# Kernel tuning notes

Hardware: AMD Instinct MI355X
Metric: run time of the kernel (lower is better)

Reference implementation:

```python
import jax, jax.numpy as jnp
import numpy as np

N = 100000
E = 800000
IN_DIM = 256
H = 4
C = 32          # per-head hidden dim
SLOPE = 0.2


def gat_conv(x, W, att_src, att_dst, bias, src, dst):
    """PyG GATConv (single input tensor => lin_src applied to both src and dst),
    concat=True, add_self_loops=False, eval mode (no attn dropout).
    x: [N, F_in], W: [H*C, F_in], att_src/att_dst: [H, C], bias: [H*C].
    Returns [N, H*C]."""
    n = x.shape[0]
    xp = (x @ W.T).reshape(n, H, C)                    # [N,H,C]
    a_src = jnp.einsum('nhc,hc->nh', xp, att_src)      # [N,H]
    a_dst = jnp.einsum('nhc,hc->nh', xp, att_dst)      # [N,H]
    e = a_src[src] + a_dst[dst]                        # [E,H]
    e = jax.nn.leaky_relu(e, SLOPE)
    # segment softmax over incoming edges of each dst node
    m = jax.ops.segment_max(e, dst, num_segments=n)    # [N,H]
    ex = jnp.exp(e - m[dst])                           # [E,H]
    s = jax.ops.segment_sum(ex, dst, num_segments=n)   # [N,H]
    alpha = ex / (s[dst] + 1e-16)                      # [E,H]
    msg = xp[src] * alpha[:, :, None]                  # [E,H,C]
    out = jax.ops.segment_sum(msg, dst, num_segments=n)  # [N,H,C]
    return out.reshape(n, H * C) + bias


def setup_inputs() -> dict:
    key = jax.random.key(0)
    ks = jax.random.split(key, 12)
    x = jax.random.normal(ks[0], (N, IN_DIM), dtype=jnp.float32)
    edge_index = jax.random.randint(ks[1], (2, E), 0, N, dtype=jnp.int64)
    g = 1.414

    def xavier(k, shape):
        fan_in, fan_out = shape[-1], int(np.prod(shape[:-1]))
        std = g * np.sqrt(2.0 / (fan_in + fan_out))
        return jax.random.normal(k, shape, dtype=jnp.float32) * std

    W0 = xavier(ks[2], (H * C, IN_DIM))
    att_src0 = xavier(ks[3], (H, C))
    att_dst0 = xavier(ks[4], (H, C))
    b0 = jnp.zeros((H * C,), dtype=jnp.float32)
    W1 = xavier(ks[5], (H * C, H * C))
    att_src1 = xavier(ks[6], (H, C))
    att_dst1 = xavier(ks[7], (H, C))
    b1 = jnp.zeros((H * C,), dtype=jnp.float32)
    return {"x": x, "edge_index": edge_index,
            "W0": W0, "att_src0": att_src0, "att_dst0": att_dst0, "b0": b0,
            "W1": W1, "att_src1": att_src1, "att_dst1": att_dst1, "b1": b1}


def reference(x, edge_index, W0, att_src0, att_dst0, b0, W1, att_src1, att_dst1, b1):
    src, dst = edge_index[0], edge_index[1]
    h = gat_conv(x, W0, att_src0, att_dst0, b0, src, dst)
    h = jax.nn.relu(h)                 # activation on all but last layer
    h = gat_conv(h, W1, att_src1, att_dst1, b1, src, dst)
    # encoding=False => no last activation; head is Identity
    return h
```

## Files before the change

### kernel.cpp

```cpp
#include <hip/hip_runtime.h>
#include <hip/hip_bf16.h>
#include <cstdint>
#include <cstddef>
#include <type_traits>

#define SLOPE 0.2f

typedef __attribute__((ext_vector_type(8))) short short8v;
typedef __attribute__((ext_vector_type(4))) float float4v;

__device__ inline ushort f2bf(float f) {
  uint u = __float_as_uint(f);
  uint r = (u + 0x7FFFu + ((u >> 16) & 1u)) >> 16;
  return (ushort)r;
}
__device__ inline float bf2f(ushort u) {
  return __uint_as_float(((uint)u) << 16);
}
__device__ inline float bflo(uint u) { return __uint_as_float(u << 16); }
__device__ inline float bfhi(uint u) { return __uint_as_float(u & 0xffff0000u); }

__device__ inline short8v pack8(float4 a, float4 b) {
  uint4 r;
  r.x = (uint)f2bf(a.x) | ((uint)f2bf(a.y) << 16);
  r.y = (uint)f2bf(a.z) | ((uint)f2bf(a.w) << 16);
  r.z = (uint)f2bf(b.x) | ((uint)f2bf(b.y) << 16);
  r.w = (uint)f2bf(b.z) | ((uint)f2bf(b.w) << 16);
  return __builtin_bit_cast(short8v, r);
}


__global__ void k_wconv(const float* __restrict__ W0, const float* __restrict__ W1,
                        ushort* __restrict__ Wb0, ushort* __restrict__ Wb1) {
  int i = blockIdx.x * 256 + threadIdx.x;
  if (i < 128 * 256) Wb0[i] = f2bf(W0[i]);
  if (i < 128 * 128) Wb1[i] = f2bf(W1[i]);
}


__global__ void k_count(const int* __restrict__ dst, int* __restrict__ counts, int E) {
  int e = blockIdx.x * 256 + threadIdx.x;
  if (e < E) atomicAdd(&counts[dst[e]], 1);
}

__global__ void k_scan1(const int* __restrict__ counts, int* __restrict__ excl,
                        int* __restrict__ bsums, int N) {
  __shared__ int lds[256];
  int tid = threadIdx.x;
  int base = blockIdx.x * 2048 + tid * 8;
  int v[8];
  int ts = 0;
#pragma unroll
  for (int i = 0; i < 8; i++) {
    int idx = base + i;
    int t = (idx < N) ? counts[idx] : 0;
    v[i] = ts;
    ts += t;
  }
  lds[tid] = ts;
  __syncthreads();
  for (int off = 1; off < 256; off <<= 1) {
    int t = (tid >= off) ? lds[tid - off] : 0;
    __syncthreads();
    lds[tid] += t;
    __syncthreads();
  }
  int texcl = (tid > 0) ? lds[tid - 1] : 0;
#pragma unroll
  for (int i = 0; i < 8; i++) {
    int idx = base + i;
    if (idx < N) excl[idx] = texcl + v[i];
  }
  if (tid == 255) bsums[blockIdx.x] = lds[255];
}

__global__ void k_scan2(int* bsums, int nb) {
  __shared__ int lds[256];
  int tid = threadIdx.x;
  int v = (tid < nb) ? bsums[tid] : 0;
  lds[tid] = v;
  __syncthreads();
  for (int off = 1; off < 256; off <<= 1) {
    int t = (tid >= off) ? lds[tid - off] : 0;
    __syncthreads();
    lds[tid] += t;
    __syncthreads();
  }
  if (tid < nb) bsums[tid] = (tid > 0) ? lds[tid - 1] : 0;
}

__global__ void k_scan3(int* __restrict__ excl, int* __restrict__ cursor,
                        const int* __restrict__ bsums, int N) {
  int tid = threadIdx.x;
  int off = bsums[blockIdx.x];
  int base = blockIdx.x * 2048 + tid * 8;
#pragma unroll
  for (int i = 0; i < 8; i++) {
    int idx = base + i;
    if (idx < N) {
      int val = excl[idx] + off;
      excl[idx] = val;
      cursor[idx] = val;
    }
  }
}

__global__ void k_fill(const int* __restrict__ src, const int* __restrict__ dst,
                       int* __restrict__ cursor,
                       int* __restrict__ src_sorted, int* __restrict__ dst_sorted,
                       int E) {
  int e = blockIdx.x * 256 + threadIdx.x;
  if (e < E) {
    int d = dst[e];
    int pos = atomicAdd(&cursor[d], 1);
    src_sorted[pos] = src[e];
    dst_sorted[pos] = d;
  }
}


template <typename AT, int K>
__global__ __launch_bounds__(256, 2) void k_gemm_lds(
    const AT* __restrict__ A, const ushort* __restrict__ Wb,
    const float* __restrict__ att_src, const float* __restrict__ att_dst,
    ushort* __restrict__ C, float* __restrict__ a_src, float* __restrict__ a_dst,
    int M) {
  constexpr int LDW = K + 8;
  __shared__ ushort Ws[128 * LDW];
  const int tid = threadIdx.x;
  const int wave = tid >> 6, lane = tid & 63;
  const int fr = lane & 15, fq = lane >> 4;
  const int bm = blockIdx.x * 128;
  const int r0 = bm + wave * 32 + fr;
  const int r1 = r0 + 16;
  const int rc0 = min(r0, M - 1), rc1 = min(r1, M - 1);

  {
    int r = tid >> 1, cb = (tid & 1) * (K / 2);
    const ushort* wp = Wb + (size_t)r * K + cb;
    ushort* dp = &Ws[r * LDW + cb];
#pragma unroll
    for (int i = 0; i < K / 16; i++)
      *(uint4*)(dp + i * 8) = *(const uint4*)(wp + i * 8);
  }
  __syncthreads();

  float4v acc[2][8] = {};
#pragma unroll
  for (int k0 = 0; k0 < K; k0 += 32) {
    short8v af0, af1;
    if constexpr (std::is_same<AT, float>::value) {
      const float* p0 = A + (size_t)rc0 * K + k0 + fq * 8;
      const float* p1 = A + (size_t)rc1 * K + k0 + fq * 8;
      af0 = pack8(*(const float4*)p0, *(const float4*)(p0 + 4));
      af1 = pack8(*(const float4*)p1, *(const float4*)(p1 + 4));
    } else {
      af0 = *(const short8v*)(A + (size_t)rc0 * K + k0 + fq * 8);
      af1 = *(const short8v*)(A + (size_t)rc1 * K + k0 + fq * 8);
    }
    short8v bfr[8];
#pragma unroll
    for (int t = 0; t < 8; t++)
      bfr[t] = *(const short8v*)&Ws[(t * 16 + fr) * LDW + k0 + fq * 8];
#pragma unroll
    for (int t = 0; t < 8; t++)
      acc[0][t] = __builtin_amdgcn_mfma_f32_16x16x32_bf16(af0, bfr[t], acc[0][t], 0, 0, 0);
#pragma unroll
    for (int t = 0; t < 8; t++)
      acc[1][t] = __builtin_amdgcn_mfma_f32_16x16x32_bf16(af1, bfr[t], acc[1][t], 0, 0, 0);
  }

  float asc[8], adc[8];
#pragma unroll
  for (int t = 0; t < 8; t++) {
    asc[t] = att_src[t * 16 + fr];
    adc[t] = att_dst[t * 16 + fr];
  }

#pragma unroll
  for (int s = 0; s < 2; s++) {
#pragma unroll
    for (int j = 0; j < 4; j++) {
      int row = bm + wave * 32 + s * 16 + fq * 4 + j;
      bool ok = row < M;
      if (ok) {
#pragma unroll
        for (int t = 0; t < 8; t++)
          C[(size_t)row * 128 + t * 16 + fr] = f2bf(acc[s][t][j]);
      }
      float ps[4], pd[4];
#pragma unroll
      for (int h = 0; h < 4; h++) {
        ps[h] = acc[s][2 * h][j] * asc[2 * h] + acc[s][2 * h + 1][j] * asc[2 * h + 1];
        pd[h] = acc[s][2 * h][j] * adc[2 * h] + acc[s][2 * h + 1][j] * adc[2 * h + 1];
      }
#pragma unroll
      for (int off = 1; off < 16; off <<= 1) {
#pragma unroll
        for (int h = 0; h < 4; h++) {
          ps[h] += __shfl_xor(ps[h], off);
          pd[h] += __shfl_xor(pd[h], off);
        }
      }
      if (ok && fr == 0) {
        *(float4*)&a_src[(size_t)row * 4] = make_float4(ps[0], ps[1], ps[2], ps[3]);
        *(float4*)&a_dst[(size_t)row * 4] = make_float4(pd[0], pd[1], pd[2], pd[3]);
      }
    }
  }
}


__global__ void k_edge(const int* __restrict__ ss, const int* __restrict__ ds,
                       const float* __restrict__ a_src, const float* __restrict__ a_dst,
                       float* __restrict__ e_sorted, int E) {
  int p = blockIdx.x * 256 + threadIdx.x;
  if (p >= E) return;
  int s = ss[p], d = ds[p];
  float4 as4 = *(const float4*)&a_src[s * 4];
  float4 ad4 = *(const float4*)&a_dst[d * 4];
  float4 ev;
  ev.x = as4.x + ad4.x; ev.x = (ev.x > 0.f) ? ev.x : SLOPE * ev.x;
  ev.y = as4.y + ad4.y; ev.y = (ev.y > 0.f) ? ev.y : SLOPE * ev.y;
  ev.z = as4.z + ad4.z; ev.z = (ev.z > 0.f) ? ev.z : SLOPE * ev.z;
  ev.w = as4.w + ad4.w; ev.w = (ev.w > 0.f) ? ev.w : SLOPE * ev.w;
  *(float4*)&e_sorted[p * 4] = ev;
}


__global__ __launch_bounds__(256) void k_msum(const float* __restrict__ e_sorted,
                                              const int* __restrict__ indptr,
                                              const int* __restrict__ counts,
                                              float* __restrict__ m_buf,
                                              float* __restrict__ inv_buf, int N) {
  int t = blockIdx.x * 256 + threadIdx.x;
  int n = t >> 2, h = t & 3;
  if (n >= N) return;
  int deg = counts[n], start = indptr[n];
  const float* eb = e_sorted + (size_t)start * 4 + h;
  float m0 = -INFINITY, m1 = -INFINITY, m2 = -INFINITY, m3 = -INFINITY;
  int i = 0;
  for (; i + 4 <= deg; i += 4) {
    float a = eb[(i + 0) * 4], b = eb[(i + 1) * 4];
    float c = eb[(i + 2) * 4], d = eb[(i + 3) * 4];
    m0 = fmaxf(m0, a); m1 = fmaxf(m1, b); m2 = fmaxf(m2, c); m3 = fmaxf(m3, d);
  }
  for (; i < deg; i++) m0 = fmaxf(m0, eb[i * 4]);
  float m = fmaxf(fmaxf(m0, m1), fmaxf(m2, m3));
  float s = 0.f;
  i = 0;
  for (; i + 4 <= deg; i += 4) {
    float a = eb[(i + 0) * 4], b = eb[(i + 1) * 4];
    float c = eb[(i + 2) * 4], d = eb[(i + 3) * 4];
    s += __expf(a - m) + __expf(b - m) + __expf(c - m) + __expf(d - m);
  }
  for (; i < deg; i++) s += __expf(eb[i * 4] - m);
  m_buf[t] = m;
  inv_buf[t] = 1.f / (s + 1e-16f);
}


template <bool RELU, typename OT>
__global__ __launch_bounds__(256) void k_agg(const ushort* __restrict__ xp,
                                             const float* __restrict__ e_sorted,
                                             const int* __restrict__ src_sorted,
                                             const int* __restrict__ indptr,
                                             const int* __restrict__ counts,
                                             const float* __restrict__ m_buf,
                                             const float* __restrict__ inv_buf,
                                             const float* __restrict__ bias,
                                             OT* __restrict__ out, int N) {
  int tid = threadIdx.x;
  int n = blockIdx.x * 8 + (tid >> 5);
  if (n >= N) return;
  int c4 = tid & 31;
  int h = c4 >> 3;
  int deg = counts[n];
  int start = indptr[n];
  const float* eb = e_sorted + (size_t)start * 4 + h;
  const int* sp = src_sorted + start;
  const ushort* xpc = xp + c4 * 4;
  float m = m_buf[n * 4 + h];
  float inv = inv_buf[n * 4 + h];

  float a0 = 0.f, a1 = 0.f, a2 = 0.f, a3 = 0.f;
  int i = 0;
  for (; i + 4 <= deg; i += 4) {
    int s0 = sp[i], s1 = sp[i + 1], s2 = sp[i + 2], s3 = sp[i + 3];
    float e0 = eb[(i + 0) * 4], e1 = eb[(i + 1) * 4];
    float e2 = eb[(i + 2) * 4], e3 = eb[(i + 3) * 4];
    uint2 v0 = *(const uint2*)(xpc + (size_t)s0 * 128);
    uint2 v1 = *(const uint2*)(xpc + (size_t)s1 * 128);
    uint2 v2 = *(const uint2*)(xpc + (size_t)s2 * 128);
    uint2 v3 = *(const uint2*)(xpc + (size_t)s3 * 128);
    float x0 = __expf(e0 - m), x1 = __expf(e1 - m);
    float x2 = __expf(e2 - m), x3 = __expf(e3 - m);
    a0 = fmaf(bflo(v0.x), x0, a0); a1 = fmaf(bfhi(v0.x), x0, a1);
    a2 = fmaf(bflo(v0.y), x0, a2); a3 = fmaf(bfhi(v0.y), x0, a3);
    a0 = fmaf(bflo(v1.x), x1, a0); a1 = fmaf(bfhi(v1.x), x1, a1);
    a2 = fmaf(bflo(v1.y), x1, a2); a3 = fmaf(bfhi(v1.y), x1, a3);
    a0 = fmaf(bflo(v2.x), x2, a0); a1 = fmaf(bfhi(v2.x), x2, a1);
    a2 = fmaf(bflo(v2.y), x2, a2); a3 = fmaf(bfhi(v2.y), x2, a3);
    a0 = fmaf(bflo(v3.x), x3, a0); a1 = fmaf(bfhi(v3.x), x3, a1);
    a2 = fmaf(bflo(v3.y), x3, a2); a3 = fmaf(bfhi(v3.y), x3, a3);
  }
  for (; i < deg; i++) {
    int s0 = sp[i];
    float x0 = __expf(eb[i * 4] - m);
    uint2 v0 = *(const uint2*)(xpc + (size_t)s0 * 128);
    a0 = fmaf(bflo(v0.x), x0, a0); a1 = fmaf(bfhi(v0.x), x0, a1);
    a2 = fmaf(bflo(v0.y), x0, a2); a3 = fmaf(bfhi(v0.y), x0, a3);
  }

  float4 bv = *(const float4*)&bias[c4 * 4];
  float o0 = fmaf(a0, inv, bv.x);
  float o1 = fmaf(a1, inv, bv.y);
  float o2 = fmaf(a2, inv, bv.z);
  float o3 = fmaf(a3, inv, bv.w);
  if (RELU) {
    o0 = fmaxf(o0, 0.f); o1 = fmaxf(o1, 0.f);
    o2 = fmaxf(o2, 0.f); o3 = fmaxf(o3, 0.f);
  }
  if constexpr (std::is_same<OT, float>::value) {
    *(float4*)&out[(size_t)n * 128 + c4 * 4] = make_float4(o0, o1, o2, o3);
  } else {
    uint2 pk;
    pk.x = (uint)f2bf(o0) | ((uint)f2bf(o1) << 16);
    pk.y = (uint)f2bf(o2) | ((uint)f2bf(o3) << 16);
    *(uint2*)&((ushort*)out)[(size_t)n * 128 + c4 * 4] = pk;
  }
}


extern "C" void kernel_launch(void* const* d_in, const int* in_sizes, int n_in,
                              void* d_out, int out_size, void* d_ws, size_t ws_size,
                              hipStream_t stream) {
  const float* x   = (const float*)d_in[0];
  const int*   ei  = (const int*)d_in[1];
  const float* W0  = (const float*)d_in[2];
  const float* as0 = (const float*)d_in[3];
  const float* ad0 = (const float*)d_in[4];
  const float* b0  = (const float*)d_in[5];
  const float* W1  = (const float*)d_in[6];
  const float* as1 = (const float*)d_in[7];
  const float* ad1 = (const float*)d_in[8];
  const float* b1  = (const float*)d_in[9];

  const int N = in_sizes[0] / 256;
  const int E = in_sizes[1] / 2;
  const int* src = ei;
  const int* dst = ei + E;

  char* ws = (char*)d_ws;
  size_t off = 0;
  auto alloc = [&](size_t bytes) -> void* {
    void* p = ws + off;
    off += (bytes + 255) & ~(size_t)255;
    return p;
  };
  ushort* xp    = (ushort*)alloc((size_t)N * 128 * 2);
  ushort* hbuf  = (ushort*)alloc((size_t)N * 128 * 2);
  float* a_src  = (float*)alloc((size_t)N * 4 * 4);
  float* a_dst  = (float*)alloc((size_t)N * 4 * 4);
  float* e_sort = (float*)alloc((size_t)E * 4 * 4);
  float* m_buf  = (float*)alloc((size_t)N * 4 * 4);
  float* i_buf  = (float*)alloc((size_t)N * 4 * 4);
  int*   counts = (int*)alloc((size_t)N * 4);
  int*   indptr = (int*)alloc((size_t)N * 4);
  int*   cursor = (int*)alloc((size_t)N * 4);
  int*   ssort  = (int*)alloc((size_t)E * 4);
  int*   dsort  = (int*)alloc((size_t)E * 4);
  int*   bsums  = (int*)alloc(256 * 4);
  ushort* Wb0   = (ushort*)alloc((size_t)128 * 256 * 2);
  ushort* Wb1   = (ushort*)alloc((size_t)128 * 128 * 2);

  hipMemsetAsync(counts, 0, (size_t)N * 4, stream);
  int eb = (E + 255) / 256;
  int nb = (N + 2047) / 2048;
  k_wconv<<<128, 256, 0, stream>>>(W0, W1, Wb0, Wb1);
  k_count<<<eb, 256, 0, stream>>>(dst, counts, E);
  k_scan1<<<nb, 256, 0, stream>>>(counts, indptr, bsums, N);
  k_scan2<<<1, 256, 0, stream>>>(bsums, nb);
  k_scan3<<<nb, 256, 0, stream>>>(indptr, cursor, bsums, N);
  k_fill<<<eb, 256, 0, stream>>>(src, dst, cursor, ssort, dsort, E);

  int gb = (N + 127) / 128;
  int mb = (N * 4 + 255) / 256;
  int gb8 = (N + 7) / 8;

  k_gemm_lds<float, 256><<<gb, 256, 0, stream>>>(x, Wb0, as0, ad0, xp,
                                                 a_src, a_dst, N);
  k_edge<<<eb, 256, 0, stream>>>(ssort, dsort, a_src, a_dst, e_sort, E);
  k_msum<<<mb, 256, 0, stream>>>(e_sort, indptr, counts, m_buf, i_buf, N);
  k_agg<true, ushort><<<gb8, 256, 0, stream>>>(xp, e_sort, ssort, indptr, counts,
                                               m_buf, i_buf, b0, hbuf, N);

  k_gemm_lds<ushort, 128><<<gb, 256, 0, stream>>>(hbuf, Wb1, as1, ad1, xp,
                                                  a_src, a_dst, N);
  k_edge<<<eb, 256, 0, stream>>>(ssort, dsort, a_src, a_dst, e_sort, E);
  k_msum<<<mb, 256, 0, stream>>>(e_sort, indptr, counts, m_buf, i_buf, N);
  k_agg<false, float><<<gb8, 256, 0, stream>>>(xp, e_sort, ssort, indptr, counts,
                                               m_buf, i_buf, b1, (float*)d_out, N);
}
```

Before: 277.3 us.

## Fuse edge-score computation into softmax and aggregation, halve GEMM weight LDS

Removes the per-edge score kernel and its E x 4 buffer. Leaky-relu edge scores are recomputed on the fly from gathered a_src and a_dst in both the max/sum kernel and the aggregation kernel, and the dst_sorted array is no longer written. The softmax-stats kernel now uses one thread per node handling all four heads, rather than one thread per node-head. The GEMM stages only 128 K-columns of weights in LDS at a time, prefetching the second half into registers and raising launch bounds to 4 blocks per CU for higher occupancy. In exchange, the softmax and aggregation kernels now do extra random gathers and recompute the scores.

```diff
diff --git a/kernel.cpp b/kernel.cpp
--- a/kernel.cpp
+++ b/kernel.cpp
@@ -28,6 +28,7 @@
   r.w = (uint)f2bf(b.z) | ((uint)f2bf(b.w) << 16);
   return __builtin_bit_cast(short8v, r);
 }
+__device__ inline float lrelu(float v) { return (v > 0.f) ? v : SLOPE * v; }
 
 
 __global__ void k_wconv(const float* __restrict__ W0, const float* __restrict__ W1,
@@ -106,26 +107,24 @@
 }
 
 __global__ void k_fill(const int* __restrict__ src, const int* __restrict__ dst,
-                       int* __restrict__ cursor,
-                       int* __restrict__ src_sorted, int* __restrict__ dst_sorted,
-                       int E) {
+                       int* __restrict__ cursor, int* __restrict__ src_sorted, int E) {
   int e = blockIdx.x * 256 + threadIdx.x;
   if (e < E) {
     int d = dst[e];
     int pos = atomicAdd(&cursor[d], 1);
     src_sorted[pos] = src[e];
-    dst_sorted[pos] = d;
   }
 }
 
 
 template <typename AT, int K>
-__global__ __launch_bounds__(256, 2) void k_gemm_lds(
+__global__ __launch_bounds__(256, 4) void k_gemm_lds(
     const AT* __restrict__ A, const ushort* __restrict__ Wb,
     const float* __restrict__ att_src, const float* __restrict__ att_dst,
     ushort* __restrict__ C, float* __restrict__ a_src, float* __restrict__ a_dst,
     int M) {
-  constexpr int LDW = K + 8;
+  constexpr int KH = 128;
+  constexpr int LDW = KH + 8;
   __shared__ ushort Ws[128 * LDW];
   const int tid = threadIdx.x;
   const int wave = tid >> 6, lane = tid & 63;
@@ -135,39 +134,60 @@
   const int r1 = r0 + 16;
   const int rc0 = min(r0, M - 1), rc1 = min(r1, M - 1);
 
-  {
-    int r = tid >> 1, cb = (tid & 1) * (K / 2);
-    const ushort* wp = Wb + (size_t)r * K + cb;
-    ushort* dp = &Ws[r * LDW + cb];
-#pragma unroll
-    for (int i = 0; i < K / 16; i++)
-      *(uint4*)(dp + i * 8) = *(const uint4*)(wp + i * 8);
-  }
+  const int sr = tid >> 1;
+  const int scb = (tid & 1) * (KH / 2);
+  const ushort* wrow = Wb + (size_t)sr * K + scb;
+  ushort* drow = &Ws[sr * LDW + scb];
+
+#pragma unroll
+  for (int i = 0; i < KH / 16; i++)
+    *(uint4*)(drow + i * 8) = *(const uint4*)(wrow + i * 8);
   __syncthreads();
 
   float4v acc[2][8] = {};
-#pragma unroll
-  for (int k0 = 0; k0 < K; k0 += 32) {
-    short8v af0, af1;
-    if constexpr (std::is_same<AT, float>::value) {
-      const float* p0 = A + (size_t)rc0 * K + k0 + fq * 8;
-      const float* p1 = A + (size_t)rc1 * K + k0 + fq * 8;
-      af0 = pack8(*(const float4*)p0, *(const float4*)(p0 + 4));
-      af1 = pack8(*(const float4*)p1, *(const float4*)(p1 + 4));
-    } else {
-      af0 = *(const short8v*)(A + (size_t)rc0 * K + k0 + fq * 8);
-      af1 = *(const short8v*)(A + (size_t)rc1 * K + k0 + fq * 8);
+
+  uint4 wreg[KH / 16];
+  if constexpr (K > KH) {
+#pragma unroll
+    for (int i = 0; i < KH / 16; i++)
+      wreg[i] = *(const uint4*)(wrow + KH + i * 8);
+  }
+
+  auto compute = [&](int kbase) {
+#pragma unroll
+    for (int k0 = 0; k0 < KH; k0 += 32) {
+      short8v af0, af1;
+      if constexpr (std::is_same<AT, float>::value) {
+        const float* p0 = A + (size_t)rc0 * K + kbase + k0 + fq * 8;
+        const float* p1 = A + (size_t)rc1 * K + kbase + k0 + fq * 8;
+        af0 = pack8(*(const float4*)p0, *(const float4*)(p0 + 4));
+        af1 = pack8(*(const float4*)p1, *(const float4*)(p1 + 4));
+      } else {
+        af0 = *(const short8v*)(A + (size_t)rc0 * K + kbase + k0 + fq * 8);
+        af1 = *(const short8v*)(A + (size_t)rc1 * K + kbase + k0 + fq * 8);
+      }
+      short8v bfr[8];
+#pragma unroll
+      for (int t = 0; t < 8; t++)
+        bfr[t] = *(const short8v*)&Ws[(t * 16 + fr) * LDW + k0 + fq * 8];
+#pragma unroll
+      for (int t = 0; t < 8; t++)
+        acc[0][t] = __builtin_amdgcn_mfma_f32_16x16x32_bf16(af0, bfr[t], acc[0][t], 0, 0, 0);
+#pragma unroll
+      for (int t = 0; t < 8; t++)
+        acc[1][t] = __builtin_amdgcn_mfma_f32_16x16x32_bf16(af1, bfr[t], acc[1][t], 0, 0, 0);
     }
-    short8v bfr[8];
-#pragma unroll
-    for (int t = 0; t < 8; t++)
-      bfr[t] = *(const short8v*)&Ws[(t * 16 + fr) * LDW + k0 + fq * 8];
-#pragma unroll
-    for (int t = 0; t < 8; t++)
-      acc[0][t] = __builtin_amdgcn_mfma_f32_16x16x32_bf16(af0, bfr[t], acc[0][t], 0, 0, 0);
-#pragma unroll
-    for (int t = 0; t < 8; t++)
-      acc[1][t] = __builtin_amdgcn_mfma_f32_16x16x32_bf16(af1, bfr[t], acc[1][t], 0, 0, 0);
+  };
+
+  compute(0);
+
+  if constexpr (K > KH) {
+    __syncthreads();
+#pragma unroll
+    for (int i = 0; i < KH / 16; i++)
+      *(uint4*)(drow + i * 8) = wreg[i];
+    __syncthreads();
+    compute(KH);
   }
 
   float asc[8], adc[8];
@@ -211,58 +231,70 @@
 }
 
 
-__global__ void k_edge(const int* __restrict__ ss, const int* __restrict__ ds,
-                       const float* __restrict__ a_src, const float* __restrict__ a_dst,
-                       float* __restrict__ e_sorted, int E) {
-  int p = blockIdx.x * 256 + threadIdx.x;
-  if (p >= E) return;
-  int s = ss[p], d = ds[p];
-  float4 as4 = *(const float4*)&a_src[s * 4];
-  float4 ad4 = *(const float4*)&a_dst[d * 4];
-  float4 ev;
-  ev.x = as4.x + ad4.x; ev.x = (ev.x > 0.f) ? ev.x : SLOPE * ev.x;
-  ev.y = as4.y + ad4.y; ev.y = (ev.y > 0.f) ? ev.y : SLOPE * ev.y;
-  ev.z = as4.z + ad4.z; ev.z = (ev.z > 0.f) ? ev.z : SLOPE * ev.z;
-  ev.w = as4.w + ad4.w; ev.w = (ev.w > 0.f) ? ev.w : SLOPE * ev.w;
-  *(float4*)&e_sorted[p * 4] = ev;
-}
-
-
-__global__ __launch_bounds__(256) void k_msum(const float* __restrict__ e_sorted,
+__global__ __launch_bounds__(256) void k_msum(const int* __restrict__ ssort,
+                                              const float* __restrict__ a_src,
+                                              const float* __restrict__ a_dst,
                                               const int* __restrict__ indptr,
                                               const int* __restrict__ counts,
                                               float* __restrict__ m_buf,
                                               float* __restrict__ inv_buf, int N) {
-  int t = blockIdx.x * 256 + threadIdx.x;
-  int n = t >> 2, h = t & 3;
+  int n = blockIdx.x * 256 + threadIdx.x;
   if (n >= N) return;
   int deg = counts[n], start = indptr[n];
-  const float* eb = e_sorted + (size_t)start * 4 + h;
-  float m0 = -INFINITY, m1 = -INFINITY, m2 = -INFINITY, m3 = -INFINITY;
+  const int* sp = ssort + start;
+  float4 ad = *(const float4*)&a_dst[(size_t)n * 4];
+
+  float4 ma = make_float4(-INFINITY, -INFINITY, -INFINITY, -INFINITY);
+  float4 mb = ma;
   int i = 0;
-  for (; i + 4 <= deg; i += 4) {
-    float a = eb[(i + 0) * 4], b = eb[(i + 1) * 4];
-    float c = eb[(i + 2) * 4], d = eb[(i + 3) * 4];
-    m0 = fmaxf(m0, a); m1 = fmaxf(m1, b); m2 = fmaxf(m2, c); m3 = fmaxf(m3, d);
-  }
-  for (; i < deg; i++) m0 = fmaxf(m0, eb[i * 4]);
-  float m = fmaxf(fmaxf(m0, m1), fmaxf(m2, m3));
-  float s = 0.f;
+  for (; i + 2 <= deg; i += 2) {
+    int s0 = sp[i], s1 = sp[i + 1];
+    float4 e0 = *(const float4*)&a_src[(size_t)s0 * 4];
+    float4 e1 = *(const float4*)&a_src[(size_t)s1 * 4];
+    ma.x = fmaxf(ma.x, lrelu(e0.x + ad.x)); ma.y = fmaxf(ma.y, lrelu(e0.y + ad.y));
+    ma.z = fmaxf(ma.z, lrelu(e0.z + ad.z)); ma.w = fmaxf(ma.w, lrelu(e0.w + ad.w));
+    mb.x = fmaxf(mb.x, lrelu(e1.x + ad.x)); mb.y = fmaxf(mb.y, lrelu(e1.y + ad.y));
+    mb.z = fmaxf(mb.z, lrelu(e1.z + ad.z)); mb.w = fmaxf(mb.w, lrelu(e1.w + ad.w));
+  }
+  for (; i < deg; i++) {
+    int s0 = sp[i];
+    float4 e0 = *(const float4*)&a_src[(size_t)s0 * 4];
+    ma.x = fmaxf(ma.x, lrelu(e0.x + ad.x)); ma.y = fmaxf(ma.y, lrelu(e0.y + ad.y));
+    ma.z = fmaxf(ma.z, lrelu(e0.z + ad.z)); ma.w = fmaxf(ma.w, lrelu(e0.w + ad.w));
+  }
+  float4 m;
+  m.x = fmaxf(ma.x, mb.x); m.y = fmaxf(ma.y, mb.y);
+  m.z = fmaxf(ma.z, mb.z); m.w = fmaxf(ma.w, mb.w);
+
+  float4 sa = make_float4(0.f, 0.f, 0.f, 0.f), sb = sa;
   i = 0;
-  for (; i + 4 <= deg; i += 4) {
-    float a = eb[(i + 0) * 4], b = eb[(i + 1) * 4];
-    float c = eb[(i + 2) * 4], d = eb[(i + 3) * 4];
-    s += __expf(a - m) + __expf(b - m) + __expf(c - m) + __expf(d - m);
-  }
-  for (; i < deg; i++) s += __expf(eb[i * 4] - m);
-  m_buf[t] = m;
-  inv_buf[t] = 1.f / (s + 1e-16f);
+  for (; i + 2 <= deg; i += 2) {
+    int s0 = sp[i], s1 = sp[i + 1];
+    float4 e0 = *(const float4*)&a_src[(size_t)s0 * 4];
+    float4 e1 = *(const float4*)&a_src[(size_t)s1 * 4];
+    sa.x += __expf(lrelu(e0.x + ad.x) - m.x); sa.y += __expf(lrelu(e0.y + ad.y) - m.y);
+    sa.z += __expf(lrelu(e0.z + ad.z) - m.z); sa.w += __expf(lrelu(e0.w + ad.w) - m.w);
+    sb.x += __expf(lrelu(e1.x + ad.x) - m.x); sb.y += __expf(lrelu(e1.y + ad.y) - m.y);
+    sb.z += __expf(lrelu(e1.z + ad.z) - m.z); sb.w += __expf(lrelu(e1.w + ad.w) - m.w);
+  }
+  for (; i < deg; i++) {
+    int s0 = sp[i];
+    float4 e0 = *(const float4*)&a_src[(size_t)s0 * 4];
+    sa.x += __expf(lrelu(e0.x + ad.x) - m.x); sa.y += __expf(lrelu(e0.y + ad.y) - m.y);
+    sa.z += __expf(lrelu(e0.z + ad.z) - m.z); sa.w += __expf(lrelu(e0.w + ad.w) - m.w);
+  }
+  float4 inv;
+  inv.x = 1.f / (sa.x + sb.x + 1e-16f); inv.y = 1.f / (sa.y + sb.y + 1e-16f);
+  inv.z = 1.f / (sa.z + sb.z + 1e-16f); inv.w = 1.f / (sa.w + sb.w + 1e-16f);
+  *(float4*)&m_buf[(size_t)n * 4] = m;
+  *(float4*)&inv_buf[(size_t)n * 4] = inv;
 }
 
 
 template <bool RELU, typename OT>
 __global__ __launch_bounds__(256) void k_agg(const ushort* __restrict__ xp,
-                                             const float* __restrict__ e_sorted,
+                                             const float* __restrict__ a_src,
+                                             const float* __restrict__ a_dst,
                                              const int* __restrict__ src_sorted,
                                              const int* __restrict__ indptr,
                                              const int* __restrict__ counts,
@@ -277,24 +309,25 @@
   int h = c4 >> 3;
   int deg = counts[n];
   int start = indptr[n];
-  const float* eb = e_sorted + (size_t)start * 4 + h;
   const int* sp = src_sorted + start;
   const ushort* xpc = xp + c4 * 4;
-  float m = m_buf[n * 4 + h];
-  float inv = inv_buf[n * 4 + h];
+  const float* asrc_h = a_src + h;
+  float ad = a_dst[(size_t)n * 4 + h];
+  float m = m_buf[(size_t)n * 4 + h];
+  float inv = inv_buf[(size_t)n * 4 + h];
 
   float a0 = 0.f, a1 = 0.f, a2 = 0.f, a3 = 0.f;
   int i = 0;
   for (; i + 4 <= deg; i += 4) {
     int s0 = sp[i], s1 = sp[i + 1], s2 = sp[i + 2], s3 = sp[i + 3];
-    float e0 = eb[(i + 0) * 4], e1 = eb[(i + 1) * 4];
-    float e2 = eb[(i + 2) * 4], e3 = eb[(i + 3) * 4];
+    float e0 = asrc_h[(size_t)s0 * 4], e1 = asrc_h[(size_t)s1 * 4];
+    float e2 = asrc_h[(size_t)s2 * 4], e3 = asrc_h[(size_t)s3 * 4];
     uint2 v0 = *(const uint2*)(xpc + (size_t)s0 * 128);
     uint2 v1 = *(const uint2*)(xpc + (size_t)s1 * 128);
     uint2 v2 = *(const uint2*)(xpc + (size_t)s2 * 128);
     uint2 v3 = *(const uint2*)(xpc + (size_t)s3 * 128);
-    float x0 = __expf(e0 - m), x1 = __expf(e1 - m);
-    float x2 = __expf(e2 - m), x3 = __expf(e3 - m);
+    float x0 = __expf(lrelu(e0 + ad) - m), x1 = __expf(lrelu(e1 + ad) - m);
+    float x2 = __expf(lrelu(e2 + ad) - m), x3 = __expf(lrelu(e3 + ad) - m);
     a0 = fmaf(bflo(v0.x), x0, a0); a1 = fmaf(bfhi(v0.x), x0, a1);
     a2 = fmaf(bflo(v0.y), x0, a2); a3 = fmaf(bfhi(v0.y), x0, a3);
     a0 = fmaf(bflo(v1.x), x1, a0); a1 = fmaf(bfhi(v1.x), x1, a1);
@@ -306,7 +339,7 @@
   }
   for (; i < deg; i++) {
     int s0 = sp[i];
-    float x0 = __expf(eb[i * 4] - m);
+    float x0 = __expf(lrelu(asrc_h[(size_t)s0 * 4] + ad) - m);
     uint2 v0 = *(const uint2*)(xpc + (size_t)s0 * 128);
     a0 = fmaf(bflo(v0.x), x0, a0); a1 = fmaf(bfhi(v0.x), x0, a1);
     a2 = fmaf(bflo(v0.y), x0, a2); a3 = fmaf(bfhi(v0.y), x0, a3);
@@ -362,14 +395,12 @@
   ushort* hbuf  = (ushort*)alloc((size_t)N * 128 * 2);
   float* a_src  = (float*)alloc((size_t)N * 4 * 4);
   float* a_dst  = (float*)alloc((size_t)N * 4 * 4);
-  float* e_sort = (float*)alloc((size_t)E * 4 * 4);
   float* m_buf  = (float*)alloc((size_t)N * 4 * 4);
   float* i_buf  = (float*)alloc((size_t)N * 4 * 4);
   int*   counts = (int*)alloc((size_t)N * 4);
   int*   indptr = (int*)alloc((size_t)N * 4);
   int*   cursor = (int*)alloc((size_t)N * 4);
   int*   ssort  = (int*)alloc((size_t)E * 4);
-  int*   dsort  = (int*)alloc((size_t)E * 4);
   int*   bsums  = (int*)alloc(256 * 4);
   ushort* Wb0   = (ushort*)alloc((size_t)128 * 256 * 2);
   ushort* Wb1   = (ushort*)alloc((size_t)128 * 128 * 2);
@@ -382,23 +413,24 @@
   k_scan1<<<nb, 256, 0, stream>>>(counts, indptr, bsums, N);
   k_scan2<<<1, 256, 0, stream>>>(bsums, nb);
   k_scan3<<<nb, 256, 0, stream>>>(indptr, cursor, bsums, N);
-  k_fill<<<eb, 256, 0, stream>>>(src, dst, cursor, ssort, dsort, E);
+  k_fill<<<eb, 256, 0, stream>>>(src, dst, cursor, ssort, E);
 
   int gb = (N + 127) / 128;
-  int mb = (N * 4 + 255) / 256;
+  int nb256 = (N + 255) / 256;
   int gb8 = (N + 7) / 8;
 
   k_gemm_lds<float, 256><<<gb, 256, 0, stream>>>(x, Wb0, as0, ad0, xp,
                                                  a_src, a_dst, N);
-  k_edge<<<eb, 256, 0, stream>>>(ssort, dsort, a_src, a_dst, e_sort, E);
-  k_msum<<<mb, 256, 0, stream>>>(e_sort, indptr, counts, m_buf, i_buf, N);
-  k_agg<true, ushort><<<gb8, 256, 0, stream>>>(xp, e_sort, ssort, indptr, counts,
-                                               m_buf, i_buf, b0, hbuf, N);
+  k_msum<<<nb256, 256, 0, stream>>>(ssort, a_src, a_dst, indptr, counts,
+                                    m_buf, i_buf, N);
+  k_agg<true, ushort><<<gb8, 256, 0, stream>>>(xp, a_src, a_dst, ssort, indptr,
+                                               counts, m_buf, i_buf, b0, hbuf, N);
 
   k_gemm_lds<ushort, 128><<<gb, 256, 0, stream>>>(hbuf, Wb1, as1, ad1, xp,
                                                   a_src, a_dst, N);
-  k_edge<<<eb, 256, 0, stream>>>(ssort, dsort, a_src, a_dst, e_sort, E);
-  k_msum<<<mb, 256, 0, stream>>>(e_sort, indptr, counts, m_buf, i_buf, N);
-  k_agg<false, float><<<gb8, 256, 0, stream>>>(xp, e_sort, ssort, indptr, counts,
-                                               m_buf, i_buf, b1, (float*)d_out, N);
-}
+  k_msum<<<nb256, 256, 0, stream>>>(ssort, a_src, a_dst, indptr, counts,
+                                    m_buf, i_buf, N);
+  k_agg<false, float><<<gb8, 256, 0, stream>>>(xp, a_src, a_dst, ssort, indptr,
+                                               counts, m_buf, i_buf, b1,
+                                               (float*)d_out, N);
+}
```

Result: slower. 295.1 us (+6.4%).
